# Performance work log

Hardware: AMD Instinct MI355X
Metric: run time of the kernel (lower is better)

## Reference

```python
import jax, jax.numpy as jnp
import numpy as np

WZ, WH, WW = 2, 6, 12          # window_size
NW = 64                        # type_of_windows = (8//2)*(96//6)
HEADS = 12
DIM = 384
B_ = 15                        # batch(1) * num_lon_windows(180//12)
N = WZ * WH * WW               # 144 tokens per window


def _construct_position_index():
    zi = np.arange(WZ); zj = -np.arange(WZ) * WZ
    hi = np.arange(WH); hj = -np.arange(WH) * WH
    w = np.arange(WW)
    c1 = np.stack(np.meshgrid(zi, hi, w, indexing='ij')).reshape(3, -1)
    c2 = np.stack(np.meshgrid(zj, hj, w, indexing='ij')).reshape(3, -1)
    coords = (c1[:, :, None] - c2[:, None, :]).transpose(1, 2, 0)  # (N, N, 3)
    coords[..., 2] += WW - 1
    coords[..., 1] *= 2 * WW - 1
    coords[..., 0] *= (2 * WW - 1) * WH * WH
    return coords.sum(-1).reshape(-1).astype(np.int32)  # (N*N,)


def setup_inputs() -> dict:
    key = jax.random.key(0)
    ks = jax.random.split(key, 6)
    bias_rows = (2 * WW - 1) * WH * WH * WZ * WZ  # 3312
    return {
        'x': jax.random.normal(ks[0], (B_, NW, N, DIM), dtype=jnp.float32),
        'mask': jnp.zeros((B_, N, N), dtype=jnp.float32),
        'w_qkv': jax.random.normal(ks[1], (DIM, 3 * DIM), dtype=jnp.float32) * 0.02,
        'b_qkv': jnp.zeros((3 * DIM,), dtype=jnp.float32),
        'w_proj': jax.random.normal(ks[2], (DIM, DIM), dtype=jnp.float32) * 0.02,
        'b_proj': jnp.zeros((DIM,), dtype=jnp.float32),
        'bias_table': jax.random.normal(ks[3], (bias_rows, NW, HEADS), dtype=jnp.float32) * 0.02,
        'position_index': jnp.asarray(_construct_position_index()),
    }


def reference(x, mask, w_qkv, b_qkv, w_proj, b_proj, bias_table, position_index):
    b_, nw, n, c = x.shape
    hd = c // HEADS
    scale = hd ** -0.5
    qkv = (x @ w_qkv + b_qkv).reshape(b_, nw, n, 3, HEADS, hd)
    q, k, v = jnp.moveaxis(qkv, 3, 0)            # each (B_, nW, N, H, hd)
    attn = jnp.einsum('bwnhd,bwmhd->bwhnm', q * scale, k)  # (B_, nW, H, N, N)
    # earth-specific relative bias gather: (N*N, nW, H) -> (nW, H, N, N)
    bias = bias_table[position_index].reshape(n, n, nw, HEADS).transpose(2, 3, 0, 1)
    attn = attn + bias[None]                     # broadcast over B_
    attn = attn + mask[:, None, None, :, :]      # additive mask per lon window
    attn = jax.nn.softmax(attn, axis=-1)         # dropout_rate=0 -> identity
    out = jnp.einsum('bwhnm,bwmhd->bwnhd', attn, v).reshape(b_, nw, n, c)
    return out @ w_proj + b_proj
```

## Files before the change

### kernel.cpp

```cpp
#include <hip/hip_runtime.h>
#include <cstdint>


typedef _Float16 f16;
typedef _Float16 f16x8 __attribute__((ext_vector_type(8)));
typedef _Float16 f16x4v __attribute__((ext_vector_type(4)));
typedef float f32x4 __attribute__((ext_vector_type(4)));

#define NW_ 64
#define HEADS_ 12
#define DIM_ 384
#define BATCH_ 15
#define NTOK_ 144
#define HD_ 32
#define MTOK_ (BATCH_*NW_*NTOK_)
#define NWH_ (BATCH_*NW_*HEADS_)

__device__ __forceinline__ void load16_lds(const void* g, void* l) {
    __builtin_amdgcn_global_load_lds(
        (const __attribute__((address_space(1))) uint32_t*)g,
        (__attribute__((address_space(3))) uint32_t*)l,
        16, 0, 0);
}

__device__ __forceinline__ f32x4 fzero4() {
    f32x4 z; z[0]=0.f; z[1]=0.f; z[2]=0.f; z[3]=0.f; return z;
}

__global__ void cvt_f32_to_f16(const float* __restrict__ src, f16* __restrict__ dst, int n4) {
    int i = blockIdx.x * blockDim.x + threadIdx.x;
    int stride = gridDim.x * blockDim.x;
    for (; i < n4; i += stride) {
        float4 v = ((const float4*)src)[i];
        f16x4v o;
        o[0] = (f16)v.x; o[1] = (f16)v.y; o[2] = (f16)v.z; o[3] = (f16)v.w;
        *(f16x4v*)(dst + 4*(size_t)i) = o;
    }
}

__global__ void transpose_cvt(const float* __restrict__ src, f16* __restrict__ dst, int K, int N) {
    int i = blockIdx.x * blockDim.x + threadIdx.x;
    if (i >= K*N) return;
    int n = i / K;
    int k = i - n*K;
    dst[i] = (f16)src[k*N + n];
}

__global__ __launch_bounds__(256) void qkv_gemm(
    const f16* __restrict__ A, const f16* __restrict__ Bt,
    const float* __restrict__ bias,
    f16* __restrict__ qws, f16* __restrict__ kws, f16* __restrict__ vws)
{
    constexpr int BK = 32;
    constexpr int NT = DIM_/BK;
    __shared__ __align__(16) f16 Asm[2][128*BK];
    __shared__ __align__(16) f16 Bsm[2][128*BK];
    const int tid  = threadIdx.x;
    const int lane = tid & 63;
    const int wave = tid >> 6;
    const int l15  = lane & 15;
    const int quad = lane >> 4;
    const int wr = wave >> 1, wc = wave & 1;

    unsigned lin = blockIdx.x;
    lin = (lin & 7u) * 1215u + (lin >> 3);
    const int row0 = (int)(lin / 9u) * 128;
    const int col0 = (int)(lin % 9u) * 128;

    f32x4 acc[4][4];
    #pragma unroll
    for (int i = 0; i < 4; ++i)
        #pragma unroll
        for (int j = 0; j < 4; ++j) acc[i][j] = fzero4();

    auto stage = [&](int kt, int b) {
        const int k0 = kt * BK;
        #pragma unroll
        for (int cc = 0; cc < 2; ++cc) {
            int chunk  = wave*2 + cc;
            int flat16 = chunk*64 + lane;
            int r   = flat16 >> 2;
            int c16 = flat16 & 3;
            load16_lds(&A [(size_t)(row0 + r)*DIM_ + k0 + c16*8], (char*)(&Asm[b][0]) + chunk*1024);
            load16_lds(&Bt[(size_t)(col0 + r)*DIM_ + k0 + c16*8], (char*)(&Bsm[b][0]) + chunk*1024);
        }
    };
    auto compute = [&](int b) {
        f16x8 af[4], bf[4];
        #pragma unroll
        for (int i = 0; i < 4; ++i)
            af[i] = *(const f16x8*)&Asm[b][(wr*64 + i*16 + l15)*BK + quad*8];
        #pragma unroll
        for (int j = 0; j < 4; ++j)
            bf[j] = *(const f16x8*)&Bsm[b][(wc*64 + j*16 + l15)*BK + quad*8];
        #pragma unroll
        for (int i = 0; i < 4; ++i)
            #pragma unroll
            for (int j = 0; j < 4; ++j)
                acc[i][j] = __builtin_amdgcn_mfma_f32_16x16x32_f16(af[i], bf[j], acc[i][j], 0, 0, 0);
    };

    stage(0, 0);
    asm volatile("s_waitcnt vmcnt(0)" ::: "memory");
    __builtin_amdgcn_s_barrier();
    __builtin_amdgcn_sched_barrier(0);
    int cur = 0;
    for (int kt = 0; kt < NT-1; ++kt) {
        stage(kt+1, cur^1);
        compute(cur);
        asm volatile("s_waitcnt vmcnt(0) lgkmcnt(0)" ::: "memory");
        __builtin_amdgcn_s_barrier();
        __builtin_amdgcn_sched_barrier(0);
        cur ^= 1;
    }
    compute(cur);

    const int which = col0 / DIM_;
    #pragma unroll
    for (int j = 0; j < 4; ++j) {
        int col = col0 + wc*64 + j*16 + l15;
        float bq = bias[col];
        int rem = col - which*DIM_;
        int h = rem >> 5, d = rem & 31;
        #pragma unroll
        for (int i = 0; i < 4; ++i) {
            int rowb = row0 + wr*64 + i*16 + quad*4;
            #pragma unroll
            for (int r = 0; r < 4; ++r) {
                int row = rowb + r;
                int bw  = row / NTOK_;
                int n   = row - bw*NTOK_;
                int head = bw*HEADS_ + h;
                f16 hv = (f16)(acc[i][j][r] + bq);
                if (which == 0)      qws[(size_t)head*NTOK_*HD_ + n*HD_ + d] = hv;
                else if (which == 1) kws[(size_t)head*NTOK_*HD_ + n*HD_ + d] = hv;
                else                 vws[(size_t)head*HD_*NTOK_ + d*NTOK_ + n] = hv;
            }
        }
    }
}

__global__ __launch_bounds__(576) void attention(
    const f16* __restrict__ qws, const f16* __restrict__ kws, const f16* __restrict__ vws,
    const float* __restrict__ bias_table, const int* __restrict__ pos_idx,
    const float* __restrict__ mask, f16* __restrict__ ows)
{
    constexpr int KPAD = 40;
    constexpr int VPAD = 168;
    __shared__ __align__(16) char smem[10752 + 48384];
    f16* Vt  = (f16*)smem;
    f16* Ksm = (f16*)(smem + 10752);
    f16* Pst = (f16*)(smem + 10752);

    const int tid  = threadIdx.x;
    const int lane = tid & 63;
    const int wv   = tid >> 6;
    const int l15  = lane & 15;
    const int quad = lane >> 4;

    const int wh = blockIdx.x;
    const int w  = wh / HEADS_;
    const int h  = wh - w*HEADS_;

    float brg[9][4];
    #pragma unroll
    for (int j = 0; j < 9; ++j) {
        int m = j*16 + l15;
        #pragma unroll
        for (int r = 0; r < 4; ++r) {
            int n = wv*16 + quad*4 + r;
            int idx = pos_idx[n*NTOK_ + m];
            brg[j][r] = bias_table[(size_t)idx*(NW_*HEADS_) + w*HEADS_ + h];
        }
    }

    if (tid < 64) {
        int d = tid >> 1, m0 = 144 + (tid & 1)*8;
        uint4 z = {0u,0u,0u,0u};
        *(uint4*)&Vt[d*VPAD + m0] = z;
    }

    const float scale = 0.17677669529663687f;

    for (int b = 0; b < BATCH_; ++b) {
        const int bwh = (b*NW_ + w)*HEADS_ + h;
        const f16* qh = qws + (size_t)bwh*NTOK_*HD_;
        const f16* kh = kws + (size_t)bwh*NTOK_*HD_;
        const f16* vh = vws + (size_t)bwh*HD_*NTOK_;

        __syncthreads();
        {
            int flat = tid*8;
            int n = flat >> 5, d = flat & 31;
            *(uint4*)&Ksm[n*KPAD + d] = *(const uint4*)&kh[flat];
            int dv = flat / NTOK_;
            int mv = flat - dv*NTOK_;
            *(uint4*)&Vt[dv*VPAD + mv] = *(const uint4*)&vh[flat];
        }
        int nq = wv*16 + l15;
        f16x8 qf = *(const f16x8*)&qh[nq*HD_ + quad*8];
        __syncthreads();

        f32x4 sfr[9];
        #pragma unroll
        for (int j = 0; j < 9; ++j) {
            f16x8 kf = *(const f16x8*)&Ksm[(j*16 + l15)*KPAD + quad*8];
            sfr[j] = __builtin_amdgcn_mfma_f32_16x16x32_f16(qf, kf, fzero4(), 0, 0, 0);
        }
        __syncthreads();

        float p[9][4], rmax[4], rsum[4];
        #pragma unroll
        for (int r = 0; r < 4; ++r) rmax[r] = -1e30f;
        const float* mrow = mask + (size_t)b*NTOK_*NTOK_;
        #pragma unroll
        for (int j = 0; j < 9; ++j) {
            int m = j*16 + l15;
            #pragma unroll
            for (int r = 0; r < 4; ++r) {
                int n = wv*16 + quad*4 + r;
                float s = sfr[j][r]*scale + brg[j][r] + mrow[n*NTOK_ + m];
                p[j][r] = s;
                rmax[r] = fmaxf(rmax[r], s);
            }
        }
        #pragma unroll
        for (int r = 0; r < 4; ++r) {
            float v = rmax[r];
            #pragma unroll
            for (int off = 1; off < 16; off <<= 1)
                v = fmaxf(v, __shfl_xor(v, off, 64));
            rmax[r] = v;
        }
        #pragma unroll
        for (int r = 0; r < 4; ++r) rsum[r] = 0.f;
        #pragma unroll
        for (int j = 0; j < 9; ++j)
            #pragma unroll
            for (int r = 0; r < 4; ++r) {
                float e = __expf(p[j][r] - rmax[r]);
                p[j][r] = e;
                rsum[r] += e;
            }
        #pragma unroll
        for (int r = 0; r < 4; ++r) {
            float v = rsum[r];
            #pragma unroll
            for (int off = 1; off < 16; off <<= 1)
                v += __shfl_xor(v, off, 64);
            rsum[r] = 1.0f / v;
        }

        f16* Pw = Pst + wv*16*VPAD;
        #pragma unroll
        for (int j = 0; j < 9; ++j) {
            int m = j*16 + l15;
            #pragma unroll
            for (int r = 0; r < 4; ++r)
                Pw[(quad*4 + r)*VPAD + m] = (f16)(p[j][r]*rsum[r]);
        }
        if (lane < 32) {
            int row = lane >> 1, m0 = 144 + (lane & 1)*8;
            uint4 z = {0u,0u,0u,0u};
            *(uint4*)&Pw[row*VPAD + m0] = z;
        }

        f32x4 o0 = fzero4(), o1 = fzero4();
        #pragma unroll
        for (int s = 0; s < 5; ++s) {
            f16x8 pa = *(const f16x8*)&Pw[l15*VPAD + s*32 + quad*8];
            f16x8 v0 = *(const f16x8*)&Vt[l15*VPAD + s*32 + quad*8];
            f16x8 v1 = *(const f16x8*)&Vt[(16 + l15)*VPAD + s*32 + quad*8];
            o0 = __builtin_amdgcn_mfma_f32_16x16x32_f16(pa, v0, o0, 0, 0, 0);
            o1 = __builtin_amdgcn_mfma_f32_16x16x32_f16(pa, v1, o1, 0, 0, 0);
        }

        const int bw = b*NW_ + w;
        #pragma unroll
        for (int r = 0; r < 4; ++r) {
            int n = wv*16 + quad*4 + r;
            size_t base = ((size_t)bw*NTOK_ + n)*DIM_ + h*HD_;
            ows[base + l15]      = (f16)o0[r];
            ows[base + 16 + l15] = (f16)o1[r];
        }
    }
}

__global__ __launch_bounds__(256) void proj_gemm(
    const f16* __restrict__ A, const f16* __restrict__ Bt,
    const float* __restrict__ bias, float* __restrict__ out)
{
    constexpr int BK = 32;
    constexpr int NT = DIM_/BK;
    __shared__ __align__(16) f16 Asm[2][128*BK];
    __shared__ __align__(16) f16 Bsm[2][128*BK];
    const int tid  = threadIdx.x;
    const int lane = tid & 63;
    const int wave = tid >> 6;
    const int l15  = lane & 15;
    const int quad = lane >> 4;
    const int wr = wave >> 1, wc = wave & 1;

    unsigned lin = blockIdx.x;
    lin = (lin & 7u) * 405u + (lin >> 3);
    const int row0 = (int)(lin / 3u) * 128;
    const int col0 = (int)(lin % 3u) * 128;

    f32x4 acc[4][4];
    #pragma unroll
    for (int i = 0; i < 4; ++i)
        #pragma unroll
        for (int j = 0; j < 4; ++j) acc[i][j] = fzero4();

    auto stage = [&](int kt, int b) {
        const int k0 = kt * BK;
        #pragma unroll
        for (int cc = 0; cc < 2; ++cc) {
            int chunk  = wave*2 + cc;
            int flat16 = chunk*64 + lane;
            int r   = flat16 >> 2;
            int c16 = flat16 & 3;
            load16_lds(&A [(size_t)(row0 + r)*DIM_ + k0 + c16*8], (char*)(&Asm[b][0]) + chunk*1024);
            load16_lds(&Bt[(size_t)(col0 + r)*DIM_ + k0 + c16*8], (char*)(&Bsm[b][0]) + chunk*1024);
        }
    };
    auto compute = [&](int b) {
        f16x8 af[4], bf[4];
        #pragma unroll
        for (int i = 0; i < 4; ++i)
            af[i] = *(const f16x8*)&Asm[b][(wr*64 + i*16 + l15)*BK + quad*8];
        #pragma unroll
        for (int j = 0; j < 4; ++j)
            bf[j] = *(const f16x8*)&Bsm[b][(wc*64 + j*16 + l15)*BK + quad*8];
        #pragma unroll
        for (int i = 0; i < 4; ++i)
            #pragma unroll
            for (int j = 0; j < 4; ++j)
                acc[i][j] = __builtin_amdgcn_mfma_f32_16x16x32_f16(af[i], bf[j], acc[i][j], 0, 0, 0);
    };

    stage(0, 0);
    asm volatile("s_waitcnt vmcnt(0)" ::: "memory");
    __builtin_amdgcn_s_barrier();
    __builtin_amdgcn_sched_barrier(0);
    int cur = 0;
    for (int kt = 0; kt < NT-1; ++kt) {
        stage(kt+1, cur^1);
        compute(cur);
        asm volatile("s_waitcnt vmcnt(0) lgkmcnt(0)" ::: "memory");
        __builtin_amdgcn_s_barrier();
        __builtin_amdgcn_sched_barrier(0);
        cur ^= 1;
    }
    compute(cur);

    #pragma unroll
    for (int j = 0; j < 4; ++j) {
        int col = col0 + wc*64 + j*16 + l15;
        float bp = bias[col];
        #pragma unroll
        for (int i = 0; i < 4; ++i) {
            int rowb = row0 + wr*64 + i*16 + quad*4;
            #pragma unroll
            for (int r = 0; r < 4; ++r)
                out[(size_t)(rowb + r)*DIM_ + col] = acc[i][j][r] + bp;
        }
    }
}

extern "C" void kernel_launch(void* const* d_in, const int* in_sizes, int n_in,
                              void* d_out, int out_size, void* d_ws, size_t ws_size,
                              hipStream_t stream)
{
    const float* x      = (const float*)d_in[0];
    const float* mask   = (const float*)d_in[1];
    const float* w_qkv  = (const float*)d_in[2];
    const float* b_qkv  = (const float*)d_in[3];
    const float* w_proj = (const float*)d_in[4];
    const float* b_proj = (const float*)d_in[5];
    const float* btab   = (const float*)d_in[6];
    const int*   pidx   = (const int*)d_in[7];
    float* out = (float*)d_out;

    constexpr size_t X16_B = (size_t)MTOK_*DIM_*2;
    constexpr size_t WTQ_B = (size_t)1152*384*2;
    constexpr size_t WTP_B = (size_t)384*384*2;
    constexpr size_t HEAD_B = (size_t)NWH_*NTOK_*HD_*2;

    char* ws = (char*)d_ws;
    f16* x16 = (f16*)ws;
    f16* wtq = (f16*)(ws + X16_B);
    f16* wtp = (f16*)(ws + X16_B + WTQ_B);
    f16* qws = (f16*)(ws + X16_B + WTQ_B + WTP_B);
    f16* kws = (f16*)((char*)qws + HEAD_B);
    f16* vws = (f16*)((char*)kws + HEAD_B);
    f16* ows = x16;

    cvt_f32_to_f16<<<8192, 256, 0, stream>>>(x, x16, MTOK_*DIM_/4);
    transpose_cvt<<<(384*1152 + 255)/256, 256, 0, stream>>>(w_qkv, wtq, 384, 1152);
    transpose_cvt<<<(384*384  + 255)/256, 256, 0, stream>>>(w_proj, wtp, 384, 384);
    qkv_gemm<<<9720, 256, 0, stream>>>(x16, wtq, b_qkv, qws, kws, vws);
    attention<<<NW_*HEADS_, 576, 0, stream>>>(qws, kws, vws, btab, pidx, mask, ows);
    proj_gemm<<<3240, 256, 0, stream>>>(ows, wtp, b_proj, out);
}
```

Measured before the change: 1.035 ms.

## Parallelize attention over batch with pre-gathered dense bias and deferred normalization

Changes the attention grid from one block per (window, head) that loops over 15 batches to one block per (batch, window, head), with a swizzled block index mapping. A new kernel gathers the relative-position bias into a dense per-(window, head) array, staged in the output buffer before the projection GEMM overwrites it, so every block reads contiguous bias instead of doing indirect gathers. Softmax normalization is moved to after the PV matmul. This targets the low occupancy of the old 768-block launch, at the cost of an extra gather kernel, a write and re-read of about 64 MB of bias, and 15x redundant bias loads.

```diff
diff --git a/kernel.cpp b/kernel.cpp
--- a/kernel.cpp
+++ b/kernel.cpp
@@ -15,6 +15,7 @@
 #define HD_ 32
 #define MTOK_ (BATCH_*NW_*NTOK_)
 #define NWH_ (BATCH_*NW_*HEADS_)
+#define NMSQ_ (NTOK_*NTOK_)
 
 __device__ __forceinline__ void load16_lds(const void* g, void* l) {
     __builtin_amdgcn_global_load_lds(
@@ -44,6 +45,16 @@
     int n = i / K;
     int k = i - n*K;
     dst[i] = (f16)src[k*N + n];
+}
+
+__global__ __launch_bounds__(256) void bias_gather(
+    const float* __restrict__ bias_table, const int* __restrict__ pos_idx,
+    float* __restrict__ dense)
+{
+    int wh = blockIdx.x;
+    int nm = blockIdx.y * 256 + threadIdx.x;
+    int idx = pos_idx[nm];
+    dense[(size_t)wh*NMSQ_ + nm] = bias_table[(size_t)idx*(NW_*HEADS_) + wh];
 }
 
 __global__ __launch_bounds__(256) void qkv_gemm(
@@ -142,7 +153,7 @@
 
 __global__ __launch_bounds__(576) void attention(
     const f16* __restrict__ qws, const f16* __restrict__ kws, const f16* __restrict__ vws,
-    const float* __restrict__ bias_table, const int* __restrict__ pos_idx,
+    const float* __restrict__ bias_dense,
     const float* __restrict__ mask, f16* __restrict__ ows)
 {
     constexpr int KPAD = 40;
@@ -158,21 +169,17 @@
     const int l15  = lane & 15;
     const int quad = lane >> 4;
 
-    const int wh = blockIdx.x;
+    unsigned bid = blockIdx.x;
+    unsigned lin = (bid & 7u) * 1440u + (bid >> 3);
+    const int wh = (int)(lin / 15u);
+    const int b  = (int)(lin - (unsigned)wh*15u);
     const int w  = wh / HEADS_;
     const int h  = wh - w*HEADS_;
 
-    float brg[9][4];
-    #pragma unroll
-    for (int j = 0; j < 9; ++j) {
-        int m = j*16 + l15;
-        #pragma unroll
-        for (int r = 0; r < 4; ++r) {
-            int n = wv*16 + quad*4 + r;
-            int idx = pos_idx[n*NTOK_ + m];
-            brg[j][r] = bias_table[(size_t)idx*(NW_*HEADS_) + w*HEADS_ + h];
-        }
-    }
+    const int bwh = b*(NW_*HEADS_) + wh;
+    const f16* qh = qws + (size_t)bwh*NTOK_*HD_;
+    const f16* kh = kws + (size_t)bwh*NTOK_*HD_;
+    const f16* vh = vws + (size_t)bwh*HD_*NTOK_;
 
     if (tid < 64) {
         int d = tid >> 1, m0 = 144 + (tid & 1)*8;
@@ -180,109 +187,112 @@
         *(uint4*)&Vt[d*VPAD + m0] = z;
     }
 
+    {
+        int flat = tid*8;
+        int n = flat >> 5, d = flat & 31;
+        *(uint4*)&Ksm[n*KPAD + d] = *(const uint4*)&kh[flat];
+        int dv = flat / NTOK_;
+        int mv = flat - dv*NTOK_;
+        *(uint4*)&Vt[dv*VPAD + mv] = *(const uint4*)&vh[flat];
+    }
+    const int nq = wv*16 + l15;
+    f16x8 qf = *(const f16x8*)&qh[nq*HD_ + quad*8];
+
+    const float* bd = bias_dense + (size_t)wh*NMSQ_;
+    float brg[9][4];
+    #pragma unroll
+    for (int j = 0; j < 9; ++j) {
+        int m = j*16 + l15;
+        #pragma unroll
+        for (int r = 0; r < 4; ++r)
+            brg[j][r] = bd[(wv*16 + quad*4 + r)*NTOK_ + m];
+    }
+
+    __syncthreads();
+
+    f32x4 sfr[9];
+    #pragma unroll
+    for (int j = 0; j < 9; ++j) {
+        f16x8 kf = *(const f16x8*)&Ksm[(j*16 + l15)*KPAD + quad*8];
+        sfr[j] = __builtin_amdgcn_mfma_f32_16x16x32_f16(qf, kf, fzero4(), 0, 0, 0);
+    }
+    __syncthreads();
+
     const float scale = 0.17677669529663687f;
 
-    for (int b = 0; b < BATCH_; ++b) {
-        const int bwh = (b*NW_ + w)*HEADS_ + h;
-        const f16* qh = qws + (size_t)bwh*NTOK_*HD_;
-        const f16* kh = kws + (size_t)bwh*NTOK_*HD_;
-        const f16* vh = vws + (size_t)bwh*HD_*NTOK_;
-
-        __syncthreads();
-        {
-            int flat = tid*8;
-            int n = flat >> 5, d = flat & 31;
-            *(uint4*)&Ksm[n*KPAD + d] = *(const uint4*)&kh[flat];
-            int dv = flat / NTOK_;
-            int mv = flat - dv*NTOK_;
-            *(uint4*)&Vt[dv*VPAD + mv] = *(const uint4*)&vh[flat];
-        }
-        int nq = wv*16 + l15;
-        f16x8 qf = *(const f16x8*)&qh[nq*HD_ + quad*8];
-        __syncthreads();
-
-        f32x4 sfr[9];
-        #pragma unroll
-        for (int j = 0; j < 9; ++j) {
-            f16x8 kf = *(const f16x8*)&Ksm[(j*16 + l15)*KPAD + quad*8];
-            sfr[j] = __builtin_amdgcn_mfma_f32_16x16x32_f16(qf, kf, fzero4(), 0, 0, 0);
-        }
-        __syncthreads();
-
-        float p[9][4], rmax[4], rsum[4];
-        #pragma unroll
-        for (int r = 0; r < 4; ++r) rmax[r] = -1e30f;
-        const float* mrow = mask + (size_t)b*NTOK_*NTOK_;
-        #pragma unroll
-        for (int j = 0; j < 9; ++j) {
-            int m = j*16 + l15;
-            #pragma unroll
-            for (int r = 0; r < 4; ++r) {
-                int n = wv*16 + quad*4 + r;
-                float s = sfr[j][r]*scale + brg[j][r] + mrow[n*NTOK_ + m];
-                p[j][r] = s;
-                rmax[r] = fmaxf(rmax[r], s);
-            }
-        }
-        #pragma unroll
-        for (int r = 0; r < 4; ++r) {
-            float v = rmax[r];
-            #pragma unroll
-            for (int off = 1; off < 16; off <<= 1)
-                v = fmaxf(v, __shfl_xor(v, off, 64));
-            rmax[r] = v;
-        }
-        #pragma unroll
-        for (int r = 0; r < 4; ++r) rsum[r] = 0.f;
-        #pragma unroll
-        for (int j = 0; j < 9; ++j)
-            #pragma unroll
-            for (int r = 0; r < 4; ++r) {
-                float e = __expf(p[j][r] - rmax[r]);
-                p[j][r] = e;
-                rsum[r] += e;
-            }
-        #pragma unroll
-        for (int r = 0; r < 4; ++r) {
-            float v = rsum[r];
-            #pragma unroll
-            for (int off = 1; off < 16; off <<= 1)
-                v += __shfl_xor(v, off, 64);
-            rsum[r] = 1.0f / v;
-        }
-
-        f16* Pw = Pst + wv*16*VPAD;
-        #pragma unroll
-        for (int j = 0; j < 9; ++j) {
-            int m = j*16 + l15;
-            #pragma unroll
-            for (int r = 0; r < 4; ++r)
-                Pw[(quad*4 + r)*VPAD + m] = (f16)(p[j][r]*rsum[r]);
-        }
-        if (lane < 32) {
-            int row = lane >> 1, m0 = 144 + (lane & 1)*8;
-            uint4 z = {0u,0u,0u,0u};
-            *(uint4*)&Pw[row*VPAD + m0] = z;
-        }
-
-        f32x4 o0 = fzero4(), o1 = fzero4();
-        #pragma unroll
-        for (int s = 0; s < 5; ++s) {
-            f16x8 pa = *(const f16x8*)&Pw[l15*VPAD + s*32 + quad*8];
-            f16x8 v0 = *(const f16x8*)&Vt[l15*VPAD + s*32 + quad*8];
-            f16x8 v1 = *(const f16x8*)&Vt[(16 + l15)*VPAD + s*32 + quad*8];
-            o0 = __builtin_amdgcn_mfma_f32_16x16x32_f16(pa, v0, o0, 0, 0, 0);
-            o1 = __builtin_amdgcn_mfma_f32_16x16x32_f16(pa, v1, o1, 0, 0, 0);
-        }
-
-        const int bw = b*NW_ + w;
+    float p[9][4], rmax[4], rsum[4];
+    #pragma unroll
+    for (int r = 0; r < 4; ++r) rmax[r] = -1e30f;
+    const float* mrow = mask + (size_t)b*NMSQ_;
+    #pragma unroll
+    for (int j = 0; j < 9; ++j) {
+        int m = j*16 + l15;
         #pragma unroll
         for (int r = 0; r < 4; ++r) {
             int n = wv*16 + quad*4 + r;
-            size_t base = ((size_t)bw*NTOK_ + n)*DIM_ + h*HD_;
-            ows[base + l15]      = (f16)o0[r];
-            ows[base + 16 + l15] = (f16)o1[r];
-        }
+            float s = sfr[j][r]*scale + brg[j][r] + mrow[n*NTOK_ + m];
+            p[j][r] = s;
+            rmax[r] = fmaxf(rmax[r], s);
+        }
+    }
+    #pragma unroll
+    for (int r = 0; r < 4; ++r) {
+        float v = rmax[r];
+        #pragma unroll
+        for (int off = 1; off < 16; off <<= 1)
+            v = fmaxf(v, __shfl_xor(v, off, 64));
+        rmax[r] = v;
+    }
+    #pragma unroll
+    for (int r = 0; r < 4; ++r) rsum[r] = 0.f;
+    #pragma unroll
+    for (int j = 0; j < 9; ++j)
+        #pragma unroll
+        for (int r = 0; r < 4; ++r) {
+            float e = __expf(p[j][r] - rmax[r]);
+            p[j][r] = e;
+            rsum[r] += e;
+        }
+    #pragma unroll
+    for (int r = 0; r < 4; ++r) {
+        float v = rsum[r];
+        #pragma unroll
+        for (int off = 1; off < 16; off <<= 1)
+            v += __shfl_xor(v, off, 64);
+        rsum[r] = 1.0f / v;
+    }
+
+    f16* Pw = Pst + wv*16*VPAD;
+    #pragma unroll
+    for (int j = 0; j < 9; ++j) {
+        int m = j*16 + l15;
+        #pragma unroll
+        for (int r = 0; r < 4; ++r)
+            Pw[(quad*4 + r)*VPAD + m] = (f16)p[j][r];
+    }
+    if (lane < 32) {
+        int row = lane >> 1, m0 = 144 + (lane & 1)*8;
+        uint4 z = {0u,0u,0u,0u};
+        *(uint4*)&Pw[row*VPAD + m0] = z;
+    }
+
+    f32x4 o0 = fzero4(), o1 = fzero4();
+    #pragma unroll
+    for (int s = 0; s < 5; ++s) {
+        f16x8 pa = *(const f16x8*)&Pw[l15*VPAD + s*32 + quad*8];
+        f16x8 v0 = *(const f16x8*)&Vt[l15*VPAD + s*32 + quad*8];
+        f16x8 v1 = *(const f16x8*)&Vt[(16 + l15)*VPAD + s*32 + quad*8];
+        o0 = __builtin_amdgcn_mfma_f32_16x16x32_f16(pa, v0, o0, 0, 0, 0);
+        o1 = __builtin_amdgcn_mfma_f32_16x16x32_f16(pa, v1, o1, 0, 0, 0);
+    }
+
+    const int bw = b*NW_ + w;
+    #pragma unroll
+    for (int r = 0; r < 4; ++r) {
+        int n = wv*16 + quad*4 + r;
+        size_t base = ((size_t)bw*NTOK_ + n)*DIM_ + h*HD_;
+        ows[base + l15]      = (f16)(o0[r]*rsum[r]);
+        ows[base + 16 + l15] = (f16)(o1[r]*rsum[r]);
     }
 }
 
@@ -396,10 +406,13 @@
     f16* vws = (f16*)((char*)kws + HEAD_B);
     f16* ows = x16;
 
+    float* bias_dense = (float*)d_out;
+
     cvt_f32_to_f16<<<8192, 256, 0, stream>>>(x, x16, MTOK_*DIM_/4);
     transpose_cvt<<<(384*1152 + 255)/256, 256, 0, stream>>>(w_qkv, wtq, 384, 1152);
     transpose_cvt<<<(384*384  + 255)/256, 256, 0, stream>>>(w_proj, wtp, 384, 384);
+    bias_gather<<<dim3(NW_*HEADS_, NMSQ_/256), 256, 0, stream>>>(btab, pidx, bias_dense);
     qkv_gemm<<<9720, 256, 0, stream>>>(x16, wtq, b_qkv, qws, kws, vws);
-    attention<<<NW_*HEADS_, 576, 0, stream>>>(qws, kws, vws, btab, pidx, mask, ows);
+    attention<<<NWH_, 576, 0, stream>>>(qws, kws, vws, bias_dense, mask, ows);
     proj_gemm<<<3240, 256, 0, stream>>>(ows, wtp, b_proj, out);
 }
```

New measurement: 1.043 ms. About the same (+0.8%).
